# Performance work log

Hardware: AMD Instinct MI355X
Metric: run time of the kernel (lower is better)

The kernel has to match this reference:

```python
import jax, jax.numpy as jnp
import numpy as np

N_NODES = 100000
N_EDGES = 1600000
IN_FEAT = 256
HIDDEN = 64
N_CLASSES = 16


def gcn_conv(x, edge_index, W, b):
    """PyG GCNConv: add self-loops, symmetric normalization, linear+aggregate."""
    n = x.shape[0]
    src, dst = edge_index[0], edge_index[1]
    loops = jnp.arange(n, dtype=src.dtype)
    src = jnp.concatenate([src, loops])
    dst = jnp.concatenate([dst, loops])
    # in-degree on graph with self-loops
    deg = jax.ops.segment_sum(jnp.ones(src.shape[0], dtype=x.dtype), dst, num_segments=n)
    dinv = jnp.where(deg > 0, jax.lax.rsqrt(deg), 0.0)
    h = x @ W                                  # [N, out]
    norm = dinv[src] * dinv[dst]               # [E+N]
    msg = h[src] * norm[:, None]                # gather + scale (memory-bound)
    out = jax.ops.segment_sum(msg, dst, num_segments=n)  # scatter-add
    return out + b


def setup_inputs() -> dict:
    key = jax.random.key(0)
    ks = jax.random.split(key, 5)
    x = jax.random.normal(ks[0], (N_NODES, IN_FEAT), dtype=jnp.float32)
    edge_index = jax.random.randint(ks[1], (2, N_EDGES), 0, N_NODES, dtype=jnp.int64)
    W1 = jax.random.normal(ks[2], (IN_FEAT, HIDDEN), dtype=jnp.float32) * (1.0 / np.sqrt(IN_FEAT))
    b1 = jnp.zeros((HIDDEN,), dtype=jnp.float32)
    W2 = jax.random.normal(ks[3], (HIDDEN, N_CLASSES), dtype=jnp.float32) * (1.0 / np.sqrt(HIDDEN))
    b2 = jnp.zeros((N_CLASSES,), dtype=jnp.float32)
    return {"x": x, "edge_index": edge_index, "W1": W1, "b1": b1, "W2": W2, "b2": b2}


def reference(x, edge_index, W1, b1, W2, b2):
    h = gcn_conv(x, edge_index, W1, b1)
    h = jax.nn.relu(h)
    # dropout p=0.5 is identity in eval mode (training=False)
    out = gcn_conv(h, edge_index, W2, b2)
    return out
```

## Files before the change

### kernel.cpp

```cpp
#include <hip/hip_runtime.h>

#define NN 100000
#define NE 1600000
#define FIN 256
#define FH 64
#define FC 16

#define SCAN_CHUNK 1024
#define NB_SCAN ((NN + SCAN_CHUNK - 1) / SCAN_CHUNK)
#define NSWEEP 2
#define SWEEP_W ((NN + NSWEEP - 1) / NSWEEP)
#define NB_COUNT ((NE + 255) / 256)
#define NB_GEMM1 ((NN + 63) / 64)
#define NB_FUSED (5 * NB_GEMM1)

typedef int v2i __attribute__((ext_vector_type(2)));

__device__ __forceinline__ float4 fma4(float4 v, float w, float4 a) {
    a.x = fmaf(v.x, w, a.x); a.y = fmaf(v.y, w, a.y);
    a.z = fmaf(v.z, w, a.z); a.w = fmaf(v.w, w, a.w);
    return a;
}
__device__ __forceinline__ float4 xor_add4(float4 r, int m) {
    r.x += __shfl_xor(r.x, m, 64); r.y += __shfl_xor(r.y, m, 64);
    r.z += __shfl_xor(r.z, m, 64); r.w += __shfl_xor(r.w, m, 64);
    return r;
}

__global__ void detect_k(const int* __restrict__ ei, int* __restrict__ flag) {
    if (threadIdx.x == 0 && blockIdx.x == 0) {
        int z = (ei[1] == 0) & (ei[3] == 0) & (ei[5] == 0) & (ei[7] == 0);
        *flag = z;
    }
}

__device__ __forceinline__ int eidx(const int* __restrict__ ei, int f, int pos) {
    return f ? ei[2 * pos] : ei[pos];
}

__global__ __launch_bounds__(256, 8) void fused_k(const int* __restrict__ ei,
                                                  const int* __restrict__ flag,
                                                  int* __restrict__ deg,
                                                  v2i* __restrict__ packed,
                                                  const float* __restrict__ x,
                                                  const float* __restrict__ W,
                                                  float* __restrict__ h) {
    __shared__ float As[32][68];
    __shared__ float Bs[32][64];
    const int b = blockIdx.x;
    if ((b % 5) != 4) {
        int cb = (b / 5) * 4 + (b % 5);
        if (cb >= NB_COUNT) return;
        int e = cb * 256 + threadIdx.x;
        if (e >= NE) return;
        int f = *flag;
        int s = eidx(ei, f, e);
        int d = eidx(ei, f, NE + e);
        int r = atomicAdd(&deg[d], 1);
        v2i p; p.x = s; p.y = d | (r << 17);
        packed[e] = p;
        return;
    }
    const int t = threadIdx.x;
    const int r0 = (b / 5) * 64;
    const int tx4 = (t & 15) * 4;
    const int ty4 = (t >> 4) * 4;
    const int xkf = (t & 7) * 4;
    const int xrow = t >> 3;
    const int wcol = (t & 15) * 4;
    const int wrow = t >> 4;

    float acc[4][4] = {};

    for (int k0 = 0; k0 < FIN; k0 += 32) {
        #pragma unroll
        for (int i = 0; i < 2; i++) {
            int row = xrow + 32 * i;
            int gr = r0 + row;
            float4 v = make_float4(0.f, 0.f, 0.f, 0.f);
            if (gr < NN) v = *(const float4*)&x[gr * FIN + k0 + xkf];
            As[xkf + 0][row] = v.x;
            As[xkf + 1][row] = v.y;
            As[xkf + 2][row] = v.z;
            As[xkf + 3][row] = v.w;
            int kr = wrow + 16 * i;
            float4 w = *(const float4*)&W[(k0 + kr) * FH + wcol];
            *(float4*)&Bs[kr][wcol] = w;
        }
        __syncthreads();
        #pragma unroll 8
        for (int kk = 0; kk < 32; kk++) {
            float4 a = *(const float4*)&As[kk][ty4];
            float4 bq = *(const float4*)&Bs[kk][tx4];
            float av[4] = {a.x, a.y, a.z, a.w};
            float bv[4] = {bq.x, bq.y, bq.z, bq.w};
            #pragma unroll
            for (int i2 = 0; i2 < 4; i2++)
                #pragma unroll
                for (int j2 = 0; j2 < 4; j2++)
                    acc[i2][j2] = fmaf(av[i2], bv[j2], acc[i2][j2]);
        }
        __syncthreads();
    }
    #pragma unroll
    for (int i2 = 0; i2 < 4; i2++) {
        int r = r0 + ty4 + i2;
        if (r < NN)
            *(float4*)&h[r * FH + tx4] =
                make_float4(acc[i2][0], acc[i2][1], acc[i2][2], acc[i2][3]);
    }
}

__global__ __launch_bounds__(256) void scan_sum_k(const int* __restrict__ deg,
                                                  int* __restrict__ partial,
                                                  float* __restrict__ dinv) {
    __shared__ int red[256];
    int b = blockIdx.x, t = threadIdx.x;
    int base = b * SCAN_CHUNK + t * 4;
    int s = 0;
    #pragma unroll
    for (int i = 0; i < 4; i++) {
        int idx = base + i;
        if (idx < NN) {
            int dv = deg[idx];
            s += dv;
            dinv[idx] = rsqrtf((float)(dv + 1));
        }
    }
    red[t] = s;
    __syncthreads();
    for (int off = 128; off > 0; off >>= 1) {
        if (t < off) red[t] += red[t + off];
        __syncthreads();
    }
    if (t == 0) partial[b] = red[0];
}

__global__ __launch_bounds__(128) void scan_part_k(int* __restrict__ partial) {
    __shared__ int s[128];
    int t = threadIdx.x;
    int v = (t < NB_SCAN) ? partial[t] : 0;
    s[t] = v; __syncthreads();
    for (int off = 1; off < 128; off <<= 1) {
        int u = (t >= off) ? s[t - off] : 0;
        __syncthreads();
        s[t] += u;
        __syncthreads();
    }
    if (t < NB_SCAN) partial[t] = s[t] - v;
}

__global__ __launch_bounds__(256) void scan_out_k(const int* __restrict__ deg,
                                                  const int* __restrict__ partial,
                                                  int* __restrict__ row_start) {
    __shared__ int s[256];
    int b = blockIdx.x, t = threadIdx.x;
    int base = b * SCAN_CHUNK + t * 4;
    int v[4]; int sum = 0;
    #pragma unroll
    for (int i = 0; i < 4; i++) {
        int idx = base + i;
        v[i] = (idx < NN) ? deg[idx] : 0;
        sum += v[i];
    }
    s[t] = sum; __syncthreads();
    for (int off = 1; off < 256; off <<= 1) {
        int u = (t >= off) ? s[t - off] : 0;
        __syncthreads();
        s[t] += u;
        __syncthreads();
    }
    int run = partial[b] + s[t] - sum;
    #pragma unroll
    for (int i = 0; i < 4; i++) {
        int idx = base + i;
        if (idx < NN) {
            row_start[idx] = run;
            run += v[i];
            if (idx == NN - 1) row_start[NN] = run;
        }
    }
}

__global__ __launch_bounds__(256) void fill_k(const v2i* __restrict__ packed,
                                              const int* __restrict__ row_start,
                                              int* __restrict__ csr,
                                              int lo, int hi) {
    int e = blockIdx.x * 256 + threadIdx.x;
    if (e >= NE) return;
    v2i p = __builtin_nontemporal_load(&packed[e]);
    int d = p.y & 0x1FFFF;
    if (d < lo || d >= hi) return;
    int r = ((unsigned)p.y) >> 17;
    csr[row_start[d] + r] = p.x;
}

__global__ __launch_bounds__(256) void agg1g_k(const int* __restrict__ csr,
                                               const int* __restrict__ row_start,
                                               const float* __restrict__ h1,
                                               const float* __restrict__ dinv,
                                               const float* __restrict__ b1,
                                               const float* __restrict__ W2,
                                               float* __restrict__ h2) {
    __shared__ float sW2[FH * FC];
    __shared__ float sp[4][FH];
    const int t = threadIdx.x;
    #pragma unroll
    for (int i = 0; i < 4; i++) sW2[t + 256 * i] = W2[t + 256 * i];
    __syncthreads();

    int wid = t >> 6;
    int n = blockIdx.x * 4 + wid;
    int lane = t & 63;
    if (n >= NN) return;
    int sg = lane >> 4;
    int fl = lane & 15;
    int s0 = row_start[n], s1 = row_start[n + 1];
    float4 A = make_float4(0.f, 0.f, 0.f, 0.f);
    float4 B = make_float4(0.f, 0.f, 0.f, 0.f);
    for (int j0 = s0; j0 < s1; j0 += 64) {
        int idx = j0 + lane;
        int sl = 0; float wl = 0.f;
        if (idx < s1) { sl = csr[idx]; wl = dinv[sl]; }
        int cnt = s1 - j0; if (cnt > 64) cnt = 64;
        int j = 0;
        for (; j + 8 <= cnt; j += 8) {
            int   eA = __shfl(sl, j + sg, 64);
            float wA = __shfl(wl, j + sg, 64);
            int   eB = __shfl(sl, j + 4 + sg, 64);
            float wB = __shfl(wl, j + 4 + sg, 64);
            float4 vA = *(const float4*)&h1[eA * FH + fl * 4];
            float4 vB = *(const float4*)&h1[eB * FH + fl * 4];
            A = fma4(vA, wA, A);
            B = fma4(vB, wB, B);
        }
        if (j + 4 <= cnt) {
            int   eA = __shfl(sl, j + sg, 64);
            float wA = __shfl(wl, j + sg, 64);
            float4 vA = *(const float4*)&h1[eA * FH + fl * 4];
            A = fma4(vA, wA, A);
            j += 4;
        }
        int rem = cnt - j;
        if (rem > 0) {
            int jj = j + (sg < rem ? sg : 0);
            int   eA = __shfl(sl, jj, 64);
            float wA = __shfl(wl, jj, 64);
            if (sg >= rem) wA = 0.f;
            float4 vA = *(const float4*)&h1[eA * FH + fl * 4];
            A = fma4(vA, wA, A);
        }
    }
    float4 r = make_float4(A.x + B.x, A.y + B.y, A.z + B.z, A.w + B.w);
    r = xor_add4(r, 16);
    r = xor_add4(r, 32);
    if (sg == 0) {
        float dn = dinv[n];
        float4 self = *(const float4*)&h1[n * FH + fl * 4];
        float4 bq = *(const float4*)&b1[fl * 4];
        float4 p;
        p.x = fmaxf(fmaf(fmaf(self.x, dn, r.x), dn, bq.x), 0.f);
        p.y = fmaxf(fmaf(fmaf(self.y, dn, r.y), dn, bq.y), 0.f);
        p.z = fmaxf(fmaf(fmaf(self.z, dn, r.z), dn, bq.z), 0.f);
        p.w = fmaxf(fmaf(fmaf(self.w, dn, r.w), dn, bq.w), 0.f);
        *(float4*)&sp[wid][fl * 4] = p;
    }
    __builtin_amdgcn_s_waitcnt(0);
    if (lane < FC) {
        float o = 0.f;
        #pragma unroll 8
        for (int k = 0; k < FH; k++)
            o = fmaf(sp[wid][k], sW2[k * FC + lane], o);
        h2[n * FC + lane] = o;
    }
}

__global__ __launch_bounds__(256) void agg2_k(const int* __restrict__ csr,
                                              const int* __restrict__ row_start,
                                              const float* __restrict__ h2,
                                              const float* __restrict__ dinv,
                                              const float* __restrict__ b2,
                                              float* __restrict__ out) {
    const int t = threadIdx.x;
    int n = blockIdx.x * 16 + (t >> 4);
    int l16 = t & 15;
    int base = t & 48;
    int q = (t >> 2) & 3;
    int c = t & 3;
    if (n >= NN) return;
    int s0 = row_start[n], s1 = row_start[n + 1];
    float4 A = make_float4(0.f, 0.f, 0.f, 0.f);
    float4 B = make_float4(0.f, 0.f, 0.f, 0.f);
    for (int j0 = s0; j0 < s1; j0 += 16) {
        int idx = j0 + l16;
        int sl = 0; float wl = 0.f;
        if (idx < s1) { sl = csr[idx]; wl = dinv[sl]; }
        int cnt = s1 - j0; if (cnt > 16) cnt = 16;
        int j = 0;
        for (; j + 8 <= cnt; j += 8) {
            int   eA = __shfl(sl, base + j + q, 64);
            float wA = __shfl(wl, base + j + q, 64);
            int   eB = __shfl(sl, base + j + 4 + q, 64);
            float wB = __shfl(wl, base + j + 4 + q, 64);
            float4 vA = *(const float4*)&h2[eA * FC + c * 4];
            float4 vB = *(const float4*)&h2[eB * FC + c * 4];
            A = fma4(vA, wA, A);
            B = fma4(vB, wB, B);
        }
        if (j + 4 <= cnt) {
            int   eA = __shfl(sl, base + j + q, 64);
            float wA = __shfl(wl, base + j + q, 64);
            float4 vA = *(const float4*)&h2[eA * FC + c * 4];
            A = fma4(vA, wA, A);
            j += 4;
        }
        int rem = cnt - j;
        if (rem > 0) {
            int jj = base + j + (q < rem ? q : 0);
            int   eA = __shfl(sl, jj, 64);
            float wA = __shfl(wl, jj, 64);
            if (q >= rem) wA = 0.f;
            float4 vA = *(const float4*)&h2[eA * FC + c * 4];
            A = fma4(vA, wA, A);
        }
    }
    float4 r = make_float4(A.x + B.x, A.y + B.y, A.z + B.z, A.w + B.w);
    r = xor_add4(r, 4);
    r = xor_add4(r, 8);
    if (q == 0) {
        float dn = dinv[n];
        float4 self = *(const float4*)&h2[n * FC + c * 4];
        float4 bq = *(const float4*)&b2[c * 4];
        float4 p;
        p.x = fmaf(fmaf(self.x, dn, r.x), dn, bq.x);
        p.y = fmaf(fmaf(self.y, dn, r.y), dn, bq.y);
        p.z = fmaf(fmaf(self.z, dn, r.z), dn, bq.z);
        p.w = fmaf(fmaf(self.w, dn, r.w), dn, bq.w);
        *(float4*)&out[n * FC + c * 4] = p;
    }
}

extern "C" void kernel_launch(void* const* d_in, const int* in_sizes, int n_in,
                              void* d_out, int out_size, void* d_ws, size_t ws_size,
                              hipStream_t stream) {
    const float* x  = (const float*)d_in[0];
    const int*   ei = (const int*)d_in[1];
    const float* W1 = (const float*)d_in[2];
    const float* b1 = (const float*)d_in[3];
    const float* W2 = (const float*)d_in[4];
    const float* b2 = (const float*)d_in[5];
    float* out = (float*)d_out;

    char* ws = (char*)d_ws;
    int*   deg       = (int*)(ws + 0);
    int*   row_start = (int*)(ws + 512 * 1024);
    float* dinv      = (float*)(ws + 1024 * 1024);
    int*   flag      = (int*)(ws + 1536 * 1024);
    int*   partial   = (int*)(ws + 1540 * 1024);
    int*   csr       = (int*)(ws + 2ull * 1024 * 1024);
    float* h1        = (float*)(ws + 9ull * 1024 * 1024);
    v2i*   packed    = (v2i*)(ws + 35ull * 1024 * 1024);
    float* h2        = (float*)(ws + 35ull * 1024 * 1024);

    detect_k<<<1, 64, 0, stream>>>(ei, flag);
    (void)hipMemsetAsync(deg, 0, NN * sizeof(int), stream);
    fused_k<<<NB_FUSED, 256, 0, stream>>>(ei, flag, deg, packed, x, W1, h1);
    scan_sum_k<<<NB_SCAN, 256, 0, stream>>>(deg, partial, dinv);
    scan_part_k<<<1, 128, 0, stream>>>(partial);
    scan_out_k<<<NB_SCAN, 256, 0, stream>>>(deg, partial, row_start);
    for (int sw = 0; sw < NSWEEP; sw++)
        fill_k<<<(NE + 255) / 256, 256, 0, stream>>>(packed, row_start, csr,
                                                     sw * SWEEP_W, (sw + 1) * SWEEP_W);

    agg1g_k<<<(NN + 3) / 4, 256, 0, stream>>>(csr, row_start, h1, dinv, b1, W2, h2);
    agg2_k<<<(NN + 15) / 16, 256, 0, stream>>>(csr, row_start, h2, dinv, b2, out);
}
```

Baseline: 361.9 us.

## Prescale features by source dinv to drop per-edge weight gathers

Pre-multiplies h1 rows by dinv in a new scale kernel and folds dinv into h2 at write time. The aggregation loops then become plain sums without gathering dinv[src] per edge. The gather loops are also unrolled to four accumulators. The two-sweep CSR fill is merged into a single pass, trading locality of the scattered writes for one fewer launch. The extra scale kernel costs one read and one write of h1.

```diff
diff --git a/kernel.cpp b/kernel.cpp
--- a/kernel.cpp
+++ b/kernel.cpp
@@ -8,8 +8,6 @@
 
 #define SCAN_CHUNK 1024
 #define NB_SCAN ((NN + SCAN_CHUNK - 1) / SCAN_CHUNK)
-#define NSWEEP 2
-#define SWEEP_W ((NN + NSWEEP - 1) / NSWEEP)
 #define NB_COUNT ((NE + 255) / 256)
 #define NB_GEMM1 ((NN + 63) / 64)
 #define NB_FUSED (5 * NB_GEMM1)
@@ -19,6 +17,10 @@
 __device__ __forceinline__ float4 fma4(float4 v, float w, float4 a) {
     a.x = fmaf(v.x, w, a.x); a.y = fmaf(v.y, w, a.y);
     a.z = fmaf(v.z, w, a.z); a.w = fmaf(v.w, w, a.w);
+    return a;
+}
+__device__ __forceinline__ float4 add4(float4 a, float4 v) {
+    a.x += v.x; a.y += v.y; a.z += v.z; a.w += v.w;
     return a;
 }
 __device__ __forceinline__ float4 xor_add4(float4 r, int m) {
@@ -136,6 +138,17 @@
     if (t == 0) partial[b] = red[0];
 }
 
+__global__ __launch_bounds__(256) void scale1_k(float* __restrict__ h1,
+                                                const float* __restrict__ dinv) {
+    int i = blockIdx.x * 256 + threadIdx.x;
+    if (i >= NN * 16) return;
+    int row = i >> 4;
+    float d = dinv[row];
+    float4 v = *(const float4*)&h1[i * 4];
+    v.x *= d; v.y *= d; v.z *= d; v.w *= d;
+    *(float4*)&h1[i * 4] = v;
+}
+
 __global__ __launch_bounds__(128) void scan_part_k(int* __restrict__ partial) {
     __shared__ int s[128];
     int t = threadIdx.x;
@@ -184,13 +197,11 @@
 
 __global__ __launch_bounds__(256) void fill_k(const v2i* __restrict__ packed,
                                               const int* __restrict__ row_start,
-                                              int* __restrict__ csr,
-                                              int lo, int hi) {
+                                              int* __restrict__ csr) {
     int e = blockIdx.x * 256 + threadIdx.x;
     if (e >= NE) return;
     v2i p = __builtin_nontemporal_load(&packed[e]);
     int d = p.y & 0x1FFFF;
-    if (d < lo || d >= hi) return;
     int r = ((unsigned)p.y) >> 17;
     csr[row_start[d] + r] = p.x;
 }
@@ -218,51 +229,60 @@
     int s0 = row_start[n], s1 = row_start[n + 1];
     float4 A = make_float4(0.f, 0.f, 0.f, 0.f);
     float4 B = make_float4(0.f, 0.f, 0.f, 0.f);
+    float4 C = make_float4(0.f, 0.f, 0.f, 0.f);
+    float4 D = make_float4(0.f, 0.f, 0.f, 0.f);
     for (int j0 = s0; j0 < s1; j0 += 64) {
         int idx = j0 + lane;
-        int sl = 0; float wl = 0.f;
-        if (idx < s1) { sl = csr[idx]; wl = dinv[sl]; }
+        int sl = (idx < s1) ? csr[idx] : 0;
         int cnt = s1 - j0; if (cnt > 64) cnt = 64;
         int j = 0;
-        for (; j + 8 <= cnt; j += 8) {
-            int   eA = __shfl(sl, j + sg, 64);
-            float wA = __shfl(wl, j + sg, 64);
-            int   eB = __shfl(sl, j + 4 + sg, 64);
-            float wB = __shfl(wl, j + 4 + sg, 64);
+        for (; j + 16 <= cnt; j += 16) {
+            int eA = __shfl(sl, j + sg, 64);
+            int eB = __shfl(sl, j + 4 + sg, 64);
+            int eC = __shfl(sl, j + 8 + sg, 64);
+            int eD = __shfl(sl, j + 12 + sg, 64);
             float4 vA = *(const float4*)&h1[eA * FH + fl * 4];
             float4 vB = *(const float4*)&h1[eB * FH + fl * 4];
-            A = fma4(vA, wA, A);
-            B = fma4(vB, wB, B);
+            float4 vC = *(const float4*)&h1[eC * FH + fl * 4];
+            float4 vD = *(const float4*)&h1[eD * FH + fl * 4];
+            A = add4(A, vA); B = add4(B, vB);
+            C = add4(C, vC); D = add4(D, vD);
+        }
+        if (j + 8 <= cnt) {
+            int eA = __shfl(sl, j + sg, 64);
+            int eB = __shfl(sl, j + 4 + sg, 64);
+            float4 vA = *(const float4*)&h1[eA * FH + fl * 4];
+            float4 vB = *(const float4*)&h1[eB * FH + fl * 4];
+            A = add4(A, vA); B = add4(B, vB);
+            j += 8;
         }
         if (j + 4 <= cnt) {
-            int   eA = __shfl(sl, j + sg, 64);
-            float wA = __shfl(wl, j + sg, 64);
+            int eA = __shfl(sl, j + sg, 64);
             float4 vA = *(const float4*)&h1[eA * FH + fl * 4];
-            A = fma4(vA, wA, A);
+            A = add4(A, vA);
             j += 4;
         }
         int rem = cnt - j;
         if (rem > 0) {
             int jj = j + (sg < rem ? sg : 0);
-            int   eA = __shfl(sl, jj, 64);
-            float wA = __shfl(wl, jj, 64);
-            if (sg >= rem) wA = 0.f;
+            int eA = __shfl(sl, jj, 64);
+            float wA = (sg < rem) ? 1.f : 0.f;
             float4 vA = *(const float4*)&h1[eA * FH + fl * 4];
             A = fma4(vA, wA, A);
         }
     }
-    float4 r = make_float4(A.x + B.x, A.y + B.y, A.z + B.z, A.w + B.w);
+    float4 r = add4(add4(A, B), add4(C, D));
     r = xor_add4(r, 16);
     r = xor_add4(r, 32);
+    float dn = dinv[n];
     if (sg == 0) {
-        float dn = dinv[n];
         float4 self = *(const float4*)&h1[n * FH + fl * 4];
         float4 bq = *(const float4*)&b1[fl * 4];
         float4 p;
-        p.x = fmaxf(fmaf(fmaf(self.x, dn, r.x), dn, bq.x), 0.f);
-        p.y = fmaxf(fmaf(fmaf(self.y, dn, r.y), dn, bq.y), 0.f);
-        p.z = fmaxf(fmaf(fmaf(self.z, dn, r.z), dn, bq.z), 0.f);
-        p.w = fmaxf(fmaf(fmaf(self.w, dn, r.w), dn, bq.w), 0.f);
+        p.x = fmaxf(fmaf(r.x + self.x, dn, bq.x), 0.f);
+        p.y = fmaxf(fmaf(r.y + self.y, dn, bq.y), 0.f);
+        p.z = fmaxf(fmaf(r.z + self.z, dn, bq.z), 0.f);
+        p.w = fmaxf(fmaf(r.w + self.w, dn, bq.w), 0.f);
         *(float4*)&sp[wid][fl * 4] = p;
     }
     __builtin_amdgcn_s_waitcnt(0);
@@ -271,7 +291,7 @@
         #pragma unroll 8
         for (int k = 0; k < FH; k++)
             o = fmaf(sp[wid][k], sW2[k * FC + lane], o);
-        h2[n * FC + lane] = o;
+        h2[n * FC + lane] = o * dn;
     }
 }
 
@@ -291,40 +311,50 @@
     int s0 = row_start[n], s1 = row_start[n + 1];
     float4 A = make_float4(0.f, 0.f, 0.f, 0.f);
     float4 B = make_float4(0.f, 0.f, 0.f, 0.f);
+    float4 C = make_float4(0.f, 0.f, 0.f, 0.f);
+    float4 D = make_float4(0.f, 0.f, 0.f, 0.f);
     for (int j0 = s0; j0 < s1; j0 += 16) {
         int idx = j0 + l16;
-        int sl = 0; float wl = 0.f;
-        if (idx < s1) { sl = csr[idx]; wl = dinv[sl]; }
+        int sl = (idx < s1) ? csr[idx] : 0;
         int cnt = s1 - j0; if (cnt > 16) cnt = 16;
         int j = 0;
-        for (; j + 8 <= cnt; j += 8) {
-            int   eA = __shfl(sl, base + j + q, 64);
-            float wA = __shfl(wl, base + j + q, 64);
-            int   eB = __shfl(sl, base + j + 4 + q, 64);
-            float wB = __shfl(wl, base + j + 4 + q, 64);
+        if (j + 16 <= cnt) {
+            int eA = __shfl(sl, base + j + q, 64);
+            int eB = __shfl(sl, base + j + 4 + q, 64);
+            int eC = __shfl(sl, base + j + 8 + q, 64);
+            int eD = __shfl(sl, base + j + 12 + q, 64);
             float4 vA = *(const float4*)&h2[eA * FC + c * 4];
             float4 vB = *(const float4*)&h2[eB * FC + c * 4];
-            A = fma4(vA, wA, A);
-            B = fma4(vB, wB, B);
+            float4 vC = *(const float4*)&h2[eC * FC + c * 4];
+            float4 vD = *(const float4*)&h2[eD * FC + c * 4];
+            A = add4(A, vA); B = add4(B, vB);
+            C = add4(C, vC); D = add4(D, vD);
+            j += 16;
+        }
+        if (j + 8 <= cnt) {
+            int eA = __shfl(sl, base + j + q, 64);
+            int eB = __shfl(sl, base + j + 4 + q, 64);
+            float4 vA = *(const float4*)&h2[eA * FC + c * 4];
+            float4 vB = *(const float4*)&h2[eB * FC + c * 4];
+            A = add4(A, vA); B = add4(B, vB);
+            j += 8;
         }
         if (j + 4 <= cnt) {
-            int   eA = __shfl(sl, base + j + q, 64);
-            float wA = __shfl(wl, base + j + q, 64);
+            int eA = __shfl(sl, base + j + q, 64);
             float4 vA = *(const float4*)&h2[eA * FC + c * 4];
-            A = fma4(vA, wA, A);
+            A = add4(A, vA);
             j += 4;
         }
         int rem = cnt - j;
         if (rem > 0) {
             int jj = base + j + (q < rem ? q : 0);
-            int   eA = __shfl(sl, jj, 64);
-            float wA = __shfl(wl, jj, 64);
-            if (q >= rem) wA = 0.f;
+            int eA = __shfl(sl, jj, 64);
+            float wA = (q < rem) ? 1.f : 0.f;
             float4 vA = *(const float4*)&h2[eA * FC + c * 4];
             A = fma4(vA, wA, A);
         }
     }
-    float4 r = make_float4(A.x + B.x, A.y + B.y, A.z + B.z, A.w + B.w);
+    float4 r = add4(add4(A, B), add4(C, D));
     r = xor_add4(r, 4);
     r = xor_add4(r, 8);
     if (q == 0) {
@@ -332,10 +362,10 @@
         float4 self = *(const float4*)&h2[n * FC + c * 4];
         float4 bq = *(const float4*)&b2[c * 4];
         float4 p;
-        p.x = fmaf(fmaf(self.x, dn, r.x), dn, bq.x);
-        p.y = fmaf(fmaf(self.y, dn, r.y), dn, bq.y);
-        p.z = fmaf(fmaf(self.z, dn, r.z), dn, bq.z);
-        p.w = fmaf(fmaf(self.w, dn, r.w), dn, bq.w);
+        p.x = fmaf(r.x + self.x, dn, bq.x);
+        p.y = fmaf(r.y + self.y, dn, bq.y);
+        p.z = fmaf(r.z + self.z, dn, bq.z);
+        p.w = fmaf(r.w + self.w, dn, bq.w);
         *(float4*)&out[n * FC + c * 4] = p;
     }
 }
@@ -366,11 +396,10 @@
     (void)hipMemsetAsync(deg, 0, NN * sizeof(int), stream);
     fused_k<<<NB_FUSED, 256, 0, stream>>>(ei, flag, deg, packed, x, W1, h1);
     scan_sum_k<<<NB_SCAN, 256, 0, stream>>>(deg, partial, dinv);
+    scale1_k<<<(NN * 16 + 255) / 256, 256, 0, stream>>>(h1, dinv);
     scan_part_k<<<1, 128, 0, stream>>>(partial);
     scan_out_k<<<NB_SCAN, 256, 0, stream>>>(deg, partial, row_start);
-    for (int sw = 0; sw < NSWEEP; sw++)
-        fill_k<<<(NE + 255) / 256, 256, 0, stream>>>(packed, row_start, csr,
-                                                     sw * SWEEP_W, (sw + 1) * SWEEP_W);
+    fill_k<<<(NE + 255) / 256, 256, 0, stream>>>(packed, row_start, csr);
 
     agg1g_k<<<(NN + 3) / 4, 256, 0, stream>>>(csr, row_start, h1, dinv, b1, W2, h2);
     agg2_k<<<(NN + 15) / 16, 256, 0, stream>>>(csr, row_start, h2, dinv, b2, out);
```

Measured after the change: 360.2 us. No clear change (-0.5%).
